# Performance work log

Hardware: AMD Instinct MI355X
Metric: run time of the kernel (lower is better)

## Reference

```python
import jax, jax.numpy as jnp
import numpy as np

IN_F = 256
OUT_F = 128
ALPHA = 0.02  # LeakyReLU negative slope
NEG_INF = -9e15


def setup_inputs() -> dict:
    key = jax.random.key(0)
    ks = jax.random.split(key, 6)
    N = 8192
    x = jax.random.normal(ks[0], (N, IN_F), dtype=jnp.float32)
    adj = jax.random.randint(ks[1], (N, N), 0, 2, dtype=jnp.int32)
    # nn.Linear(in_feature, out_feature)
    lim1 = 1.0 / np.sqrt(IN_F)
    W1 = jax.random.uniform(ks[2], (IN_F, OUT_F), minval=-lim1, maxval=lim1, dtype=jnp.float32)
    b1 = jax.random.uniform(ks[3], (OUT_F,), minval=-lim1, maxval=lim1, dtype=jnp.float32)
    # nn.Linear(2*out_feature, 1)
    lim2 = 1.0 / np.sqrt(2 * OUT_F)
    a = jax.random.uniform(ks[4], (2 * OUT_F,), minval=-lim2, maxval=lim2, dtype=jnp.float32)
    b_att = jax.random.uniform(ks[5], (), minval=-lim2, maxval=lim2, dtype=jnp.float32)
    return {"x": x, "adj": adj, "W1": W1, "b1": b1, "a": a, "b_att": b_att}


def reference(x, adj, W1, b1, a, b_att):
    # Wh = weight1(x)  -> [N, F_out]
    Wh = x @ W1 + b1
    # att(cat(Wh_i, Wh_j)) = Wh_i @ a[:F] + Wh_j @ a[F:] + b  (no N^2*2F tensor)
    f_src = Wh @ a[:OUT_F]   # [N]
    f_dst = Wh @ a[OUT_F:]   # [N]
    e = f_src[:, None] + f_dst[None, :] + b_att          # [N, N]
    e = jnp.where(e > 0, e, ALPHA * e)                    # LeakyReLU
    scores = jnp.where(adj > 0, e, NEG_INF)
    attention = jax.nn.softmax(scores, axis=1)            # [N, N]
    # dropout is identity in eval mode (training=False)
    h_prime = attention @ Wh                               # [N, F_out]
    return jax.nn.elu(h_prime)                             # concat=True
```

## Files before the change

kernel.cpp:

```cpp
#include <hip/hip_runtime.h>
#include <hip/hip_bf16.h>

#define NODES 8192
#define INF_ 256
#define OUTF 128
#define LRALPHA 0.02f

typedef __bf16 bf16;
typedef bf16 bf16x8 __attribute__((ext_vector_type(8)));
typedef float f32x4 __attribute__((ext_vector_type(4)));
typedef float f32x16 __attribute__((ext_vector_type(16)));
typedef int i32x4 __attribute__((ext_vector_type(4)));

__global__ __launch_bounds__(256) void gat_pack_r6(
    const int* __restrict__ adj, unsigned long long* __restrict__ mask)
{
    const int lane = threadIdx.x & 63;
    const size_t W = ((size_t)blockIdx.x * 256 + threadIdx.x) >> 6;
    const size_t base = W * 512;
    int v[8];
#pragma unroll
    for (int e = 0; e < 8; ++e) v[e] = adj[base + (size_t)e * 64 + lane];
#pragma unroll
    for (int e = 0; e < 8; ++e) {
        unsigned long long b = __ballot(v[e] != 0);
        if (lane == e) mask[W * 8 + e] = b;
    }
}

__global__ __launch_bounds__(256) void gat_prep_r6(
    const float* __restrict__ x, const float* __restrict__ W1,
    const float* __restrict__ b1, const float* __restrict__ a,
    const float* __restrict__ b_att,
    bf16* __restrict__ WhbF, float* __restrict__ E1,
    float* __restrict__ E2, float* __restrict__ F1, float* __restrict__ F2)
{
    __shared__ float xsT[64][36];
    __shared__ float ws1[64][132];
    __shared__ float wh[32][128];

    const int t = threadIdx.x;
    const int rbase = blockIdx.x * 32;
    const int tr = t >> 5;
    const int tc = t & 31;

    f32x4 acc[4];
    f32x4 bias = *(const f32x4*)&b1[tc * 4];
#pragma unroll
    for (int i = 0; i < 4; ++i) acc[i] = bias;

    for (int kt = 0; kt < 4; ++kt) {
        const int kb = kt * 64;
        {
            int r = t >> 3;
            int kq = (t & 7) * 8;
            f32x4 v0 = *(const f32x4*)&x[(size_t)(rbase + r) * INF_ + kb + kq];
            f32x4 v1 = *(const f32x4*)&x[(size_t)(rbase + r) * INF_ + kb + kq + 4];
#pragma unroll
            for (int i = 0; i < 4; ++i) xsT[kq + i][r] = v0[i];
#pragma unroll
            for (int i = 0; i < 4; ++i) xsT[kq + 4 + i][r] = v1[i];
        }
        {
            int kr = t >> 2;
            int cq = (t & 3) * 32;
#pragma unroll
            for (int i = 0; i < 8; ++i) {
                f32x4 v = *(const f32x4*)&W1[(size_t)(kb + kr) * OUTF + cq + i * 4];
                *(f32x4*)&ws1[kr][cq + i * 4] = v;
            }
        }
        __syncthreads();
        for (int kk = 0; kk < 64; ++kk) {
            f32x4 xa = *(const f32x4*)&xsT[kk][tr * 4];
            f32x4 wb = *(const f32x4*)&ws1[kk][tc * 4];
#pragma unroll
            for (int i = 0; i < 4; ++i)
#pragma unroll
                for (int j = 0; j < 4; ++j)
                    acc[i][j] += xa[i] * wb[j];
        }
        __syncthreads();
    }

#pragma unroll
    for (int i = 0; i < 4; ++i)
        *(f32x4*)&wh[tr * 4 + i][tc * 4] = acc[i];
    __syncthreads();

    if (t < 32) {
        float s1 = 0.f, s2 = 0.f;
        for (int c = 0; c < OUTF; ++c) {
            float v = wh[t][c];
            s1 += v * a[c];
            s2 += v * a[OUTF + c];
        }
        float fsv = s1 + b_att[0];
        int r = rbase + t;
        E1[r] = expf(fsv);
        E2[r] = expf(LRALPHA * fsv);
        F1[r] = expf(s2);
        F2[r] = expf(LRALPHA * s2);
    }

    {
        const int kb = t >> 7;
        const int fb = (t >> 5) & 3;
        const int c  = t & 31;
        const size_t jblk = (size_t)blockIdx.x * 2 + kb;
#pragma unroll
        for (int h = 0; h < 2; ++h) {
            const int lane = c + h * 32;
            bf16x8 v;
#pragma unroll
            for (int e = 0; e < 8; ++e)
                v[e] = (bf16)wh[kb * 16 + h * 8 + e][fb * 32 + c];
            *(bf16x8*)&WhbF[((jblk * 4 + fb) * 64 + lane) * 8] = v;
        }
    }
}

#define DENRED_OFF 0
#define TAB_OFF    2048
#define ZONE_OFF   2048
#define SMEM2_SIZE 133120

__global__ __launch_bounds__(1024, 4) void gat_attn_r6(
    const unsigned int* __restrict__ m32,
    const bf16* __restrict__ WhbF,
    const float* __restrict__ E1, const float* __restrict__ E2,
    const float* __restrict__ F1, const float* __restrict__ F2,
    float* __restrict__ out)
{
    extern __shared__ char smem[];
    float* denred = (float*)(smem + DENRED_OFF);
    float* F1t = (float*)(smem + TAB_OFF);
    float* F2t = (float*)(smem + TAB_OFF + 32768);

    const int tid = threadIdx.x;
    const int lane = tid & 63;
    const int wv = tid >> 6;
    const int rbase = blockIdx.x * 32;
    const int r = lane & 31;
    const int ag = lane >> 5;
    const int agsh = ag * 8;

    {
        int i = tid * 8;
        *(f32x4*)&F1t[i]     = *(const f32x4*)&F1[i];
        *(f32x4*)&F1t[i + 4] = *(const f32x4*)&F1[i + 4];
        *(f32x4*)&F2t[i]     = *(const f32x4*)&F2[i];
        *(f32x4*)&F2t[i + 4] = *(const f32x4*)&F2[i + 4];
    }

    const float e1v = E1[rbase + r];
    const float e2v = E2[rbase + r];
    const int j0 = wv * 512;
    const size_t mrow = (size_t)(rbase + r) * 256 + wv * 16;

    f32x16 acc0, acc1, acc2, acc3;
#pragma unroll
    for (int i = 0; i < 16; ++i) { acc0[i] = 0.f; acc1[i] = 0.f; acc2[i] = 0.f; acc3[i] = 0.f; }
    float den = 0.f;

    __syncthreads();

    auto run16 = [&](i32x4 ma, i32x4 mb, int sbase) {
#pragma unroll
        for (int s2 = 0; s2 < 16; ++s2) {
            const int s = sbase + s2;
            const size_t fbase = ((size_t)(wv * 32 + s) * 4) * 512 + lane * 8;
            bf16x8 wc0 = *(const bf16x8*)&WhbF[fbase];
            bf16x8 wc1 = *(const bf16x8*)&WhbF[fbase + 512];
            bf16x8 wc2 = *(const bf16x8*)&WhbF[fbase + 1024];
            bf16x8 wc3 = *(const bf16x8*)&WhbF[fbase + 1536];

            const int jl = j0 + s * 16 + agsh;
            f32x4 g1a = *(const f32x4*)&F1t[jl];
            f32x4 g1b = *(const f32x4*)&F1t[jl + 4];
            f32x4 g2a = *(const f32x4*)&F2t[jl];
            f32x4 g2b = *(const f32x4*)&F2t[jl + 4];

            const unsigned int word =
                ((s2 >> 1) < 4) ? (unsigned int)ma[(s2 >> 1) & 3]
                                : (unsigned int)mb[(s2 >> 1) & 3];
            const unsigned int b8 = word >> (((s2 & 1) << 4) + agsh);

            bf16x8 wb;
#pragma unroll
            for (int jj = 0; jj < 4; ++jj) {
                float tv = e1v * g1a[jj];
                float w = tv > 1.f ? tv : e2v * g2a[jj];
                w = (b8 & (1u << jj)) ? w : 0.f;
                den += w;
                wb[jj] = (bf16)w;
            }
#pragma unroll
            for (int jj = 0; jj < 4; ++jj) {
                float tv = e1v * g1b[jj];
                float w = tv > 1.f ? tv : e2v * g2b[jj];
                w = (b8 & (16u << jj)) ? w : 0.f;
                den += w;
                wb[4 + jj] = (bf16)w;
            }

            acc0 = __builtin_amdgcn_mfma_f32_32x32x16_bf16(wc0, wb, acc0, 0, 0, 0);
            acc1 = __builtin_amdgcn_mfma_f32_32x32x16_bf16(wc1, wb, acc1, 0, 0, 0);
            acc2 = __builtin_amdgcn_mfma_f32_32x32x16_bf16(wc2, wb, acc2, 0, 0, 0);
            acc3 = __builtin_amdgcn_mfma_f32_32x32x16_bf16(wc3, wb, acc3, 0, 0, 0);
        }
    };

    {
        i32x4 mA = *(const i32x4*)&m32[mrow];
        i32x4 mB = *(const i32x4*)&m32[mrow + 4];
        run16(mA, mB, 0);
    }
    {
        i32x4 mC = *(const i32x4*)&m32[mrow + 8];
        i32x4 mD = *(const i32x4*)&m32[mrow + 12];
        run16(mC, mD, 16);
    }

    den += __shfl_xor(den, 32);

    __syncthreads();
    if (lane < 32) denred[wv * 32 + r] = den;

    auto dump = [&](int slot) {
        float* z = (float*)(smem + ZONE_OFF + (size_t)slot * 16384) + lane * 64;
        *(f32x16*)(z)      = acc0;
        *(f32x16*)(z + 16) = acc1;
        *(f32x16*)(z + 32) = acc2;
        *(f32x16*)(z + 48) = acc3;
    };
    auto take = [&](int slot) {
        const float* z = (const float*)(smem + ZONE_OFF + (size_t)slot * 16384) + lane * 64;
        f32x16 v0 = *(const f32x16*)(z);
        f32x16 v1 = *(const f32x16*)(z + 16);
        f32x16 v2 = *(const f32x16*)(z + 32);
        f32x16 v3 = *(const f32x16*)(z + 48);
#pragma unroll
        for (int i = 0; i < 16; ++i) {
            acc0[i] += v0[i]; acc1[i] += v1[i]; acc2[i] += v2[i]; acc3[i] += v3[i];
        }
    };

    if (wv >= 8) dump(wv - 8);
    __syncthreads();
    if (wv < 8) take(wv);
    __syncthreads();
    if (wv >= 4 && wv < 8) dump(wv - 4);
    __syncthreads();
    if (wv < 4) take(wv);
    __syncthreads();
    if (wv == 2 || wv == 3) dump(wv - 2);
    __syncthreads();
    if (wv < 2) take(wv);
    __syncthreads();
    if (wv == 1) dump(0);
    __syncthreads();

    if (wv == 0) {
        take(0);
        float ds = 0.f;
#pragma unroll
        for (int w = 0; w < 16; ++w) ds += denred[w * 32 + r];
        const float inv = 1.f / ds;
        const size_t orow = (size_t)(rbase + r) * OUTF;
#pragma unroll
        for (int fb = 0; fb < 4; ++fb) {
            const f32x16* A = (fb == 0) ? &acc0 : (fb == 1) ? &acc1 : (fb == 2) ? &acc2 : &acc3;
#pragma unroll
            for (int u = 0; u < 4; ++u) {
                f32x4 o;
#pragma unroll
                for (int e = 0; e < 4; ++e) {
                    float v = (*A)[4 * u + e] * inv;
                    o[e] = v > 0.f ? v : expm1f(v);
                }
                *(f32x4*)&out[orow + fb * 32 + 8 * u + 4 * ag] = o;
            }
        }
    }
}

extern "C" void kernel_launch(void* const* d_in, const int* in_sizes, int n_in,
                              void* d_out, int out_size, void* d_ws, size_t ws_size,
                              hipStream_t stream) {
    const float* x     = (const float*)d_in[0];
    const int*   adj   = (const int*)d_in[1];
    const float* W1    = (const float*)d_in[2];
    const float* b1    = (const float*)d_in[3];
    const float* a     = (const float*)d_in[4];
    const float* b_att = (const float*)d_in[5];
    float* out = (float*)d_out;

    char* ws = (char*)d_ws;
    unsigned long long* mask = (unsigned long long*)ws;
    bf16* WhbF = (bf16*)(ws + (size_t)8 * 1024 * 1024);
    float* E1 = (float*)(ws + (size_t)10 * 1024 * 1024);
    float* E2 = E1 + NODES;
    float* F1 = E2 + NODES;
    float* F2 = F1 + NODES;

    hipLaunchKernelGGL(gat_pack_r6, dim3(32768), dim3(256), 0, stream, adj, mask);

    hipLaunchKernelGGL(gat_prep_r6, dim3(NODES / 32), dim3(256), 0, stream,
                       x, W1, b1, a, b_att, WhbF, E1, E2, F1, F2);

    hipLaunchKernelGGL(gat_attn_r6, dim3(NODES / 32), dim3(1024), SMEM2_SIZE, stream,
                       (const unsigned int*)mask, WhbF, E1, E2, F1, F2, out);
}
```

Baseline: 126.3 us.

## Fuse adjacency bit-packing into attention kernel with software-prefetched ballots

Removes the separate pack kernel and its mask round-trip through global memory. The attention kernel now reads the int32 adjacency rows directly, packs them into bitmasks with wave ballots, and prefetches the next 64-column chunk while running the MFMAs on the current one. The reduction scratch slots are also padded (stride 65) to reduce LDS bank conflicts. In exchange the kernel carries 32 extra registers for prefetched adjacency values, which may pressure occupancy, and its 256 MB adjacency read now sits on the attention kernel's critical path.

```diff
diff --git a/kernel.cpp b/kernel.cpp
--- a/kernel.cpp
+++ b/kernel.cpp
@@ -12,23 +12,7 @@
 typedef float f32x16 __attribute__((ext_vector_type(16)));
 typedef int i32x4 __attribute__((ext_vector_type(4)));
 
-__global__ __launch_bounds__(256) void gat_pack_r6(
-    const int* __restrict__ adj, unsigned long long* __restrict__ mask)
-{
-    const int lane = threadIdx.x & 63;
-    const size_t W = ((size_t)blockIdx.x * 256 + threadIdx.x) >> 6;
-    const size_t base = W * 512;
-    int v[8];
-#pragma unroll
-    for (int e = 0; e < 8; ++e) v[e] = adj[base + (size_t)e * 64 + lane];
-#pragma unroll
-    for (int e = 0; e < 8; ++e) {
-        unsigned long long b = __ballot(v[e] != 0);
-        if (lane == e) mask[W * 8 + e] = b;
-    }
-}
-
-__global__ __launch_bounds__(256) void gat_prep_r6(
+__global__ __launch_bounds__(256) void gat_prep_r9(
     const float* __restrict__ x, const float* __restrict__ W1,
     const float* __restrict__ b1, const float* __restrict__ a,
     const float* __restrict__ b_att,
@@ -123,10 +107,11 @@
 #define DENRED_OFF 0
 #define TAB_OFF    2048
 #define ZONE_OFF   2048
-#define SMEM2_SIZE 133120
-
-__global__ __launch_bounds__(1024, 4) void gat_attn_r6(
-    const unsigned int* __restrict__ m32,
+#define SLOT_BYTES 16640
+#define SMEM2_SIZE (2048 + 8 * SLOT_BYTES)
+
+__global__ __launch_bounds__(1024, 4) void gat_attn_r9(
+    const int* __restrict__ adj,
     const bf16* __restrict__ WhbF,
     const float* __restrict__ E1, const float* __restrict__ E2,
     const float* __restrict__ F1, const float* __restrict__ F2,
@@ -156,7 +141,7 @@
     const float e1v = E1[rbase + r];
     const float e2v = E2[rbase + r];
     const int j0 = wv * 512;
-    const size_t mrow = (size_t)(rbase + r) * 256 + wv * 16;
+    const size_t adj_base = (size_t)rbase * NODES + j0 + lane;
 
     f32x16 acc0, acc1, acc2, acc3;
 #pragma unroll
@@ -165,10 +150,30 @@
 
     __syncthreads();
 
-    auto run16 = [&](i32x4 ma, i32x4 mb, int sbase) {
-#pragma unroll
-        for (int s2 = 0; s2 < 16; ++s2) {
-            const int s = sbase + s2;
+    unsigned long long myb = 0ull;
+    {
+        int av[32];
+#pragma unroll
+        for (int q = 0; q < 32; ++q)
+            av[q] = adj[adj_base + (size_t)q * NODES];
+#pragma unroll
+        for (int q = 0; q < 32; ++q) {
+            unsigned long long b = __ballot(av[q] != 0);
+            myb = (q == r) ? b : myb;
+        }
+    }
+
+#pragma unroll 1
+    for (int cb = 0; cb < 8; ++cb) {
+        const int cbn = (cb < 7) ? (cb + 1) : 7;
+        int av[32];
+#pragma unroll
+        for (int q = 0; q < 32; ++q)
+            av[q] = adj[adj_base + (size_t)q * NODES + cbn * 64];
+
+#pragma unroll
+        for (int i16 = 0; i16 < 4; ++i16) {
+            const int s = cb * 4 + i16;
             const size_t fbase = ((size_t)(wv * 32 + s) * 4) * 512 + lane * 8;
             bf16x8 wc0 = *(const bf16x8*)&WhbF[fbase];
             bf16x8 wc1 = *(const bf16x8*)&WhbF[fbase + 512];
@@ -181,10 +186,8 @@
             f32x4 g2a = *(const f32x4*)&F2t[jl];
             f32x4 g2b = *(const f32x4*)&F2t[jl + 4];
 
-            const unsigned int word =
-                ((s2 >> 1) < 4) ? (unsigned int)ma[(s2 >> 1) & 3]
-                                : (unsigned int)mb[(s2 >> 1) & 3];
-            const unsigned int b8 = word >> (((s2 & 1) << 4) + agsh);
+            const unsigned int b8 =
+                (unsigned int)(myb >> (i16 * 16 + agsh)) & 0xffu;
 
             bf16x8 wb;
 #pragma unroll
@@ -209,17 +212,14 @@
             acc2 = __builtin_amdgcn_mfma_f32_32x32x16_bf16(wc2, wb, acc2, 0, 0, 0);
             acc3 = __builtin_amdgcn_mfma_f32_32x32x16_bf16(wc3, wb, acc3, 0, 0, 0);
         }
-    };
-
-    {
-        i32x4 mA = *(const i32x4*)&m32[mrow];
-        i32x4 mB = *(const i32x4*)&m32[mrow + 4];
-        run16(mA, mB, 0);
-    }
-    {
-        i32x4 mC = *(const i32x4*)&m32[mrow + 8];
-        i32x4 mD = *(const i32x4*)&m32[mrow + 12];
-        run16(mC, mD, 16);
+
+        if (cb < 7) {
+#pragma unroll
+            for (int q = 0; q < 32; ++q) {
+                unsigned long long b = __ballot(av[q] != 0);
+                myb = (q == r) ? b : myb;
+            }
+        }
     }
 
     den += __shfl_xor(den, 32);
@@ -228,14 +228,14 @@
     if (lane < 32) denred[wv * 32 + r] = den;
 
     auto dump = [&](int slot) {
-        float* z = (float*)(smem + ZONE_OFF + (size_t)slot * 16384) + lane * 64;
+        float* z = (float*)(smem + ZONE_OFF + (size_t)slot * SLOT_BYTES) + lane * 65;
         *(f32x16*)(z)      = acc0;
         *(f32x16*)(z + 16) = acc1;
         *(f32x16*)(z + 32) = acc2;
         *(f32x16*)(z + 48) = acc3;
     };
     auto take = [&](int slot) {
-        const float* z = (const float*)(smem + ZONE_OFF + (size_t)slot * 16384) + lane * 64;
+        const float* z = (const float*)(smem + ZONE_OFF + (size_t)slot * SLOT_BYTES) + lane * 65;
         f32x16 v0 = *(const f32x16*)(z);
         f32x16 v1 = *(const f32x16*)(z + 16);
         f32x16 v2 = *(const f32x16*)(z + 32);
@@ -297,18 +297,15 @@
     float* out = (float*)d_out;
 
     char* ws = (char*)d_ws;
-    unsigned long long* mask = (unsigned long long*)ws;
-    bf16* WhbF = (bf16*)(ws + (size_t)8 * 1024 * 1024);
-    float* E1 = (float*)(ws + (size_t)10 * 1024 * 1024);
+    bf16* WhbF = (bf16*)ws;
+    float* E1 = (float*)(ws + (size_t)2 * 1024 * 1024);
     float* E2 = E1 + NODES;
     float* F1 = E2 + NODES;
     float* F2 = F1 + NODES;
 
-    hipLaunchKernelGGL(gat_pack_r6, dim3(32768), dim3(256), 0, stream, adj, mask);
-
-    hipLaunchKernelGGL(gat_prep_r6, dim3(NODES / 32), dim3(256), 0, stream,
+    hipLaunchKernelGGL(gat_prep_r9, dim3(NODES / 32), dim3(256), 0, stream,
                        x, W1, b1, a, b_att, WhbF, E1, E2, F1, F2);
 
-    hipLaunchKernelGGL(gat_attn_r6, dim3(NODES / 32), dim3(1024), SMEM2_SIZE, stream,
-                       (const unsigned int*)mask, WhbF, E1, E2, F1, F2, out);
+    hipLaunchKernelGGL(gat_attn_r9, dim3(NODES / 32), dim3(1024), SMEM2_SIZE, stream,
+                       adj, WhbF, E1, E2, F1, F2, out);
 }
```

Result: slower. 348.5 us (+176.0%).
